# Optimization experiments

Hardware: AMD Instinct MI355X
Metric: run time of the kernel (lower is better)

The kernel has to match this reference:

```python
import jax, jax.numpy as jnp
import numpy as np

B, T, H = 2, 2048, 1024
EXPAND, N = 2, 16
DIN = H * EXPAND  # 2048
EPS = 1e-6


def rmsnorm(x, w):
    var = jnp.mean(x * x, axis=-1, keepdims=True)
    return x * jax.lax.rsqrt(var + EPS) * w


def setup_inputs() -> dict:
    key = jax.random.key(0)
    ks = jax.random.split(key, 9)
    s_h = 1.0 / np.sqrt(H)
    s_d = 1.0 / np.sqrt(DIN)
    return {
        "x": jax.random.normal(ks[0], (B, T, H), jnp.float32),
        "norm_w": jnp.ones((H,), jnp.float32),
        "in_proj_w": jax.random.normal(ks[1], (H, 2 * DIN), jnp.float32) * s_h,
        "A_proj_w": jax.random.normal(ks[2], (DIN, DIN), jnp.float32) * s_d,
        "A_proj_b": jax.random.normal(ks[3], (DIN,), jnp.float32) * 0.02,
        "A_base": jnp.log(jnp.arange(1, N + 1, dtype=jnp.float32)),
        "B_proj_w": jax.random.normal(ks[4], (DIN, N), jnp.float32) * s_d,
        "C_proj_w": jax.random.normal(ks[5], (DIN, N), jnp.float32) * s_d,
        "D": jnp.ones((DIN,), jnp.float32),
        "out_proj_w": jax.random.normal(ks[6], (DIN, H), jnp.float32) * s_d,
    }


def liquid_scan(x_in, a_mod, a_base, B_in, C_in):
    # x_in, a_mod: [B,T,DIN]; B_in, C_in: [B,T,N]; a_base: [N]
    def step(h, inp):
        a_t, b_t, c_t, x_t = inp  # [B,DIN], [B,N], [B,N], [B,DIN]
        # h: [B, DIN, N]
        h = (a_t[:, :, None] * a_base) * h + b_t[:, None, :] * x_t[:, :, None]
        y_t = jnp.einsum('bdn,bn->bd', h, c_t)
        return h, y_t

    h0 = jnp.zeros((x_in.shape[0], DIN, N), x_in.dtype)
    xs = (jnp.swapaxes(a_mod, 0, 1), jnp.swapaxes(B_in, 0, 1),
          jnp.swapaxes(C_in, 0, 1), jnp.swapaxes(x_in, 0, 1))
    _, ys = jax.lax.scan(step, h0, xs)  # ys: [T,B,DIN]
    return jnp.swapaxes(ys, 0, 1)


def reference(x, norm_w, in_proj_w, A_proj_w, A_proj_b, A_base, B_proj_w, C_proj_w, D, out_proj_w):
    residual = x
    xn = rmsnorm(x, norm_w)
    xz = xn @ in_proj_w                      # [B,T,2*DIN]
    x_in, z = jnp.split(xz, 2, axis=-1)
    x_in = jax.nn.silu(x_in)
    a_mod = jax.nn.sigmoid(x_in @ A_proj_w + A_proj_b)  # [B,T,DIN]
    a_base = jax.nn.sigmoid(A_base)                      # [N]
    B_in = x_in @ B_proj_w                               # [B,T,N]
    C_in = x_in @ C_proj_w                               # [B,T,N]
    y = liquid_scan(x_in, a_mod, a_base, B_in, C_in)     # [B,T,DIN]
    y = (y + D * x_in) * jax.nn.silu(z)
    return residual + y @ out_proj_w
```

## Files before the change

kernel.cpp:

```cpp
#include <hip/hip_runtime.h>
#include <hip/hip_fp16.h>
#include <cstdint>

#define B_    2
#define T_    2048
#define H_    1024
#define DIN_  2048
#define NS_   16
#define M_    (B_*T_)
#define NCHUNK 64
#define LCHUNK 32

using bf16x8 = __attribute__((ext_vector_type(8))) short;
using f32x4  = __attribute__((ext_vector_type(4))) float;

__device__ __forceinline__ unsigned short f2bf(float f) {
    union { float f; uint32_t u; } x; x.f = f;
    uint32_t u = x.u;
    uint32_t r = (u + 0x7fffu + ((u >> 16) & 1u)) >> 16;
    return (unsigned short)r;
}
__device__ __forceinline__ float bf2f(unsigned short h) {
    union { uint32_t u; float f; } x; x.u = ((uint32_t)h) << 16;
    return x.f;
}
__device__ __forceinline__ float sigm(float v) { return 1.0f / (1.0f + expf(-v)); }
__device__ __forceinline__ float silu(float v) { return v / (1.0f + expf(-v)); }

__device__ __forceinline__ void gload_lds16(const void* g, void* l) {
    __builtin_amdgcn_global_load_lds(
        (__attribute__((address_space(1))) void*)(void*)g,
        (__attribute__((address_space(3))) void*)l, 16, 0, 0);
}

__global__ __launch_bounds__(256)
void prep_all(const float* __restrict__ in_proj, const float* __restrict__ A_proj,
              const float* __restrict__ out_proj,
              const float* __restrict__ x, const float* __restrict__ norm_w,
              unsigned short* __restrict__ inT, unsigned short* __restrict__ W2,
              unsigned short* __restrict__ outT, unsigned short* __restrict__ xnh) {
    int bid = blockIdx.x;
    int tid = threadIdx.x;
    __shared__ float tile[32][33];
    __shared__ float red[4];
    if (bid >= 10240) {
        int row = bid - 10240;
        const float4* xr = (const float4*)(x + (size_t)row * H_);
        float4 v = xr[tid];
        float ss = v.x * v.x + v.y * v.y + v.z * v.z + v.w * v.w;
#pragma unroll
        for (int o = 32; o > 0; o >>= 1) ss += __shfl_down(ss, o, 64);
        int lane = tid & 63, wv = tid >> 6;
        if (lane == 0) red[wv] = ss;
        __syncthreads();
        float tot = red[0] + red[1] + red[2] + red[3];
        float rstd = rsqrtf(tot / (float)H_ + 1e-6f);
        const float4* wr = (const float4*)norm_w;
        float4 w4 = wr[tid];
        size_t o = (size_t)row * H_ + tid * 4;
        *(ushort4*)&xnh[o] = make_ushort4(f2bf(v.x * rstd * w4.x), f2bf(v.y * rstd * w4.y),
                                          f2bf(v.z * rstd * w4.z), f2bf(v.w * rstd * w4.w));
        return;
    }
    const float* src; unsigned short* dst; int K, N, l;
    if (bid < 4096)      { src = in_proj;  dst = inT;  K = 1024; N = 4096; l = bid; }
    else if (bid < 8192) { src = A_proj;   dst = W2;   K = 2048; N = 2048; l = bid - 4096; }
    else                 { src = out_proj; dst = outT; K = 2048; N = 1024; l = bid - 8192; }
    int ntiles = N >> 5;
    int n0 = (l % ntiles) * 32, k0 = (l / ntiles) * 32;
    int tx = tid & 31, ty = tid >> 5;
#pragma unroll
    for (int i = 0; i < 32; i += 8)
        tile[ty + i][tx] = src[(size_t)(k0 + ty + i) * N + (n0 + tx)];
    __syncthreads();
    int sx = (tid & 15) * 2;
    int sy = tid >> 4;
#pragma unroll
    for (int i = 0; i < 32; i += 16) {
        int n = sy + i;
        float v0 = tile[sx][n], v1 = tile[sx + 1][n];
        size_t o = (size_t)(n0 + n) * K + (k0 + sx);
        *(ushort2*)&dst[o] = make_ushort2(f2bf(v0), f2bf(v1));
    }
}

template <int EPI, int BM, int BN>
__global__ __launch_bounds__(512, (BM == 128) ? 4 : 2)
void gemm8p(const unsigned short* __restrict__ Aa, const unsigned short* __restrict__ Bw,
            int K,
            float* __restrict__ out0,
            unsigned short* __restrict__ oh, unsigned short* __restrict__ oz,
            const float* __restrict__ aux, __half* __restrict__ oha) {
    constexpr int AU   = (BM / 16) * 2;
    constexpr int BU   = (BN / 16) * 2;
    constexpr int BUFU = AU + BU;
    constexpr int MF   = BM / 2 / 16;
    constexpr int NF   = BN / 4 / 16;
    constexpr int PH   = (NF == 4) ? 2 : 1;
    constexpr int NP   = NF / PH;
    constexpr int SPWK = BUFU / 8;
    constexpr int SPG  = SPWK / 2;
    constexpr int SPP  = SPG / PH;
    __shared__ unsigned short sm[2 * BUFU * 512];
    const int tid  = threadIdx.x;
    const int lane = tid & 63;
    const int wid  = tid >> 6;
    const int wm   = wid >> 2;
    const int wn   = wid & 3;

    const int gx   = gridDim.x;
    const int nwg  = gx * gridDim.y;
    const int orig = blockIdx.y * gx + blockIdx.x;
    const int qq   = nwg >> 3;
    const int lid  = (orig & 7) * qq + (orig >> 3);
    const int bm   = (lid / gx) * BM;
    const int bn   = (lid % gx) * BN;

    const int srow  = lane >> 2;
    const int sgran = (lane & 3) ^ ((lane >> 3) & 3);
    const unsigned short* gpp[SPWK];
    int lofs_[SPWK];
#pragma unroll
    for (int g = 0; g < 2; ++g)
#pragma unroll
        for (int i = 0; i < SPG; ++i) {
            int cn = wid * SPG + i;
            const unsigned short* src;
            int u;
            if (cn < AU / 2) { u = cn * 2 + g;             src = Aa + (size_t)(bm + cn * 16 + srow) * K; }
            else { int bc = cn - AU / 2; u = AU + bc * 2 + g; src = Bw + (size_t)(bn + bc * 16 + srow) * K; }
            gpp[g * SPG + i]   = src + g * 32 + sgran * 8;
            lofs_[g * SPG + i] = u * 512;
        }

    const int nt = K >> 6;
#pragma unroll
    for (int j = 0; j < SPWK; ++j) gload_lds16(gpp[j], &sm[lofs_[j]]);

    const int fro = (lane & 15) * 32 + (((lane >> 4) ^ ((lane >> 1) & 3)) * 8);

    f32x4 acc[MF][NF] = {};
    for (int kt = 0; kt < nt; ++kt) {
        const unsigned short* sb = &sm[(kt & 1) * (BUFU * 512)];
        unsigned short*       db = &sm[((kt + 1) & 1) * (BUFU * 512)];
        const bool pf = (kt + 1 < nt);
        bf16x8 af[MF];
#pragma unroll
        for (int ks = 0; ks < 2; ++ks) {
            if (ks == 1 && kt == nt - 1) {
                asm volatile("s_waitcnt vmcnt(0)" ::: "memory");
            } else {
                if constexpr (SPG == 4)      asm volatile("s_waitcnt vmcnt(4)" ::: "memory");
                else if constexpr (SPG == 3) asm volatile("s_waitcnt vmcnt(3)" ::: "memory");
                else                         asm volatile("s_waitcnt vmcnt(2)" ::: "memory");
            }
            __builtin_amdgcn_s_barrier();
            __builtin_amdgcn_sched_barrier(0);
#pragma unroll
            for (int ph = 0; ph < PH; ++ph) {
                if (ph) {
                    __builtin_amdgcn_s_barrier();
                    __builtin_amdgcn_sched_barrier(0);
                }
                if (ph == 0) {
#pragma unroll
                    for (int mf = 0; mf < MF; ++mf)
                        af[mf] = *(const bf16x8*)&sb[((wm * MF + mf) * 2 + ks) * 512 + fro];
                }
                bf16x8 bf8[NP];
#pragma unroll
                for (int j = 0; j < NP; ++j) {
                    int nfg = ph * NP + j;
                    bf8[j] = *(const bf16x8*)&sb[(AU + (wn * NF + nfg) * 2 + ks) * 512 + fro];
                }
                if (pf) {
#pragma unroll
                    for (int j = 0; j < SPP; ++j) {
                        int s = (ks * PH + ph) * SPP + j;
                        gload_lds16(gpp[s] + (size_t)(kt + 1) * 64, db + lofs_[s]);
                    }
                }
                __builtin_amdgcn_s_setprio(1);
#pragma unroll
                for (int mf = 0; mf < MF; ++mf)
#pragma unroll
                    for (int j = 0; j < NP; ++j)
                        acc[mf][ph * NP + j] = __builtin_amdgcn_mfma_f32_16x16x32_bf16(
                            af[mf], bf8[j], acc[mf][ph * NP + j], 0, 0, 0);
                __builtin_amdgcn_s_setprio(0);
            }
        }
    }

#pragma unroll
    for (int mf = 0; mf < MF; ++mf)
#pragma unroll
        for (int nf = 0; nf < NF; ++nf) {
            int col  = bn + (wn * NF + nf) * 16 + (lane & 15);
            int row0 = bm + (wm * MF + mf) * 16 + ((lane >> 4) << 2);
#pragma unroll
            for (int r = 0; r < 4; ++r) {
                int row = row0 + r;
                float v = acc[mf][nf][r];
                if (EPI == 0) {
                    float s = silu(v);
                    if (col < DIN_) oh[(size_t)row * DIN_ + col] = f2bf(s);
                    else            oz[(size_t)row * DIN_ + (col - DIN_)] = f2bf(s);
                } else if (EPI == 1) {
                    oha[(size_t)row * DIN_ + col] = __float2half(sigm(v + aux[col]));
                } else {
                    out0[(size_t)row * H_ + col] = v + aux[(size_t)row * H_ + col];
                }
            }
        }
}

#define KT_ 512
__global__ __launch_bounds__(256)
void bc_proj(const unsigned short* __restrict__ xh,
             const float* __restrict__ Bw, const float* __restrict__ Cw,
             float* __restrict__ Bout, float* __restrict__ Cout) {
    __shared__ float wB[KT_][17];
    __shared__ float wC[KT_][17];
    const int m0  = blockIdx.x * 16;
    const int tid = threadIdx.x;
    const int r   = tid >> 4;
    const int j   = tid & 15;
    float ab[16], ac[16];
#pragma unroll
    for (int i = 0; i < 16; ++i) { ab[i] = 0.f; ac[i] = 0.f; }

    for (int kt = 0; kt < DIN_; kt += KT_) {
        if (kt) __syncthreads();
        const float4* bs = (const float4*)(Bw + (size_t)kt * 16);
        const float4* cs = (const float4*)(Cw + (size_t)kt * 16);
#pragma unroll
        for (int i = 0; i < 8; ++i) {
            int idx = i * 256 + tid;
            int kk = idx >> 2, c4 = (idx & 3) * 4;
            float4 vb = bs[idx], vc = cs[idx];
            wB[kk][c4 + 0] = vb.x; wB[kk][c4 + 1] = vb.y; wB[kk][c4 + 2] = vb.z; wB[kk][c4 + 3] = vb.w;
            wC[kk][c4 + 0] = vc.x; wC[kk][c4 + 1] = vc.y; wC[kk][c4 + 2] = vc.z; wC[kk][c4 + 3] = vc.w;
        }
        __syncthreads();
        const unsigned short* xr = xh + (size_t)(m0 + r) * DIN_ + kt;
#pragma unroll 4
        for (int kk = 0; kk < 32; ++kk) {
            int kl = kk * 16 + j;
            float x = bf2f(xr[kl]);
#pragma unroll
            for (int c = 0; c < 16; ++c) {
                ab[c] = fmaf(x, wB[kl][c], ab[c]);
                ac[c] = fmaf(x, wC[kl][c], ac[c]);
            }
        }
    }
#pragma unroll
    for (int i = 0; i < 16; ++i) {
#pragma unroll
        for (int m = 8; m > 0; m >>= 1) {
            ab[i] += __shfl_xor(ab[i], m, 64);
            ac[i] += __shfl_xor(ac[i], m, 64);
        }
    }
    if (j == 0) {
#pragma unroll
        for (int i = 0; i < 16; ++i) {
            Bout[(size_t)(m0 + r) * 16 + i] = ab[i];
            Cout[(size_t)(m0 + r) * 16 + i] = ac[i];
        }
    }
}

__global__ __launch_bounds__(256)
void scan_phase1(const __half* __restrict__ amod, const unsigned short* __restrict__ xh,
                 const float* __restrict__ Bin, const float* __restrict__ Abase,
                 float* __restrict__ P, float* __restrict__ S) {
    int d = blockIdx.x * 256 + threadIdx.x;
    int c = blockIdx.y;
    int b = blockIdx.z;
    float ab[16];
#pragma unroll
    for (int n = 0; n < 16; ++n) ab[n] = sigm(Abase[n]);
    float p[16], s[16];
#pragma unroll
    for (int n = 0; n < 16; ++n) { p[n] = 1.0f; s[n] = 0.0f; }
    int t0 = c * LCHUNK;
    for (int tt = 0; tt < LCHUNK; ++tt) {
        size_t mrow = (size_t)(b * T_ + t0 + tt);
        float a = __half2float(amod[mrow * DIN_ + d]);
        float x = bf2f(xh[mrow * DIN_ + d]);
        const float4* bt4 = (const float4*)(Bin + mrow * 16);
        float4 q0 = bt4[0], q1 = bt4[1], q2 = bt4[2], q3 = bt4[3];
        float bt[16];
        bt[0]=q0.x; bt[1]=q0.y; bt[2]=q0.z; bt[3]=q0.w;
        bt[4]=q1.x; bt[5]=q1.y; bt[6]=q1.z; bt[7]=q1.w;
        bt[8]=q2.x; bt[9]=q2.y; bt[10]=q2.z; bt[11]=q2.w;
        bt[12]=q3.x; bt[13]=q3.y; bt[14]=q3.z; bt[15]=q3.w;
#pragma unroll
        for (int n = 0; n < 16; ++n) {
            float dk = a * ab[n];
            p[n] *= dk;
            s[n] = fmaf(dk, s[n], bt[n] * x);
        }
    }
    size_t base = ((size_t)(b * NCHUNK + c) << 15) + (size_t)d * 16;
    float4* P4 = (float4*)(P + base);
    float4* S4 = (float4*)(S + base);
#pragma unroll
    for (int j = 0; j < 4; ++j) {
        P4[j] = make_float4(p[4*j], p[4*j+1], p[4*j+2], p[4*j+3]);
        S4[j] = make_float4(s[4*j], s[4*j+1], s[4*j+2], s[4*j+3]);
    }
}

__global__ __launch_bounds__(256)
void scan_phase2(const float* __restrict__ P, const float* __restrict__ S,
                 float* __restrict__ H0) {
    int idx = blockIdx.x * 256 + threadIdx.x;
    int b = idx >> 15;
    int dn = idx & 32767;
    float g = 0.f;
    for (int c = 0; c < NCHUNK; ++c) {
        size_t base = ((size_t)(b * NCHUNK + c) << 15) + dn;
        H0[base] = g;
        g = fmaf(P[base], g, S[base]);
    }
}

__global__ __launch_bounds__(256)
void scan_phase3(const __half* __restrict__ amod, const unsigned short* __restrict__ xh,
                 const float* __restrict__ Bin, const float* __restrict__ Cin,
                 const float* __restrict__ Abase, const float* __restrict__ H0,
                 const float* __restrict__ Dp, const unsigned short* __restrict__ szh,
                 unsigned short* __restrict__ yh) {
    int d = blockIdx.x * 256 + threadIdx.x;
    int c = blockIdx.y;
    int b = blockIdx.z;
    float ab[16];
#pragma unroll
    for (int n = 0; n < 16; ++n) ab[n] = sigm(Abase[n]);
    float h[16];
    size_t hbase = ((size_t)(b * NCHUNK + c) << 15) + (size_t)d * 16;
    const float4* H4 = (const float4*)(H0 + hbase);
#pragma unroll
    for (int j = 0; j < 4; ++j) {
        float4 t4 = H4[j];
        h[j*4] = t4.x; h[j*4+1] = t4.y; h[j*4+2] = t4.z; h[j*4+3] = t4.w;
    }
    float Dd = Dp[d];
    int t0 = c * LCHUNK;
    for (int tt = 0; tt < LCHUNK; ++tt) {
        size_t mrow = (size_t)(b * T_ + t0 + tt);
        float a = __half2float(amod[mrow * DIN_ + d]);
        float x = bf2f(xh[mrow * DIN_ + d]);
        const float4* bt4 = (const float4*)(Bin + mrow * 16);
        const float4* ct4 = (const float4*)(Cin + mrow * 16);
        float4 q0 = bt4[0], q1 = bt4[1], q2 = bt4[2], q3 = bt4[3];
        float4 r0 = ct4[0], r1 = ct4[1], r2 = ct4[2], r3 = ct4[3];
        float bt[16], ct[16];
        bt[0]=q0.x; bt[1]=q0.y; bt[2]=q0.z; bt[3]=q0.w;
        bt[4]=q1.x; bt[5]=q1.y; bt[6]=q1.z; bt[7]=q1.w;
        bt[8]=q2.x; bt[9]=q2.y; bt[10]=q2.z; bt[11]=q2.w;
        bt[12]=q3.x; bt[13]=q3.y; bt[14]=q3.z; bt[15]=q3.w;
        ct[0]=r0.x; ct[1]=r0.y; ct[2]=r0.z; ct[3]=r0.w;
        ct[4]=r1.x; ct[5]=r1.y; ct[6]=r1.z; ct[7]=r1.w;
        ct[8]=r2.x; ct[9]=r2.y; ct[10]=r2.z; ct[11]=r2.w;
        ct[12]=r3.x; ct[13]=r3.y; ct[14]=r3.z; ct[15]=r3.w;
        float y = 0.f;
#pragma unroll
        for (int n = 0; n < 16; ++n) {
            float dk = a * ab[n];
            h[n] = fmaf(dk, h[n], bt[n] * x);
            y = fmaf(h[n], ct[n], y);
        }
        float val = (y + Dd * x) * bf2f(szh[mrow * DIN_ + d]);
        yh[mrow * DIN_ + d] = f2bf(val);
    }
}

extern "C" void kernel_launch(void* const* d_in, const int* in_sizes, int n_in,
                              void* d_out, int out_size, void* d_ws, size_t ws_size,
                              hipStream_t stream) {
    const float* x          = (const float*)d_in[0];
    const float* norm_w     = (const float*)d_in[1];
    const float* in_proj_w  = (const float*)d_in[2];
    const float* A_proj_w   = (const float*)d_in[3];
    const float* A_proj_b   = (const float*)d_in[4];
    const float* A_base     = (const float*)d_in[5];
    const float* B_proj_w   = (const float*)d_in[6];
    const float* C_proj_w   = (const float*)d_in[7];
    const float* Dp         = (const float*)d_in[8];
    const float* out_proj_w = (const float*)d_in[9];
    float* out = (float*)d_out;

    char* ws = (char*)d_ws;
    size_t off = 0;
    auto alloc = [&](size_t bytes) -> char* {
        char* p = ws + off;
        off += (bytes + 255) & ~(size_t)255;
        return p;
    };
    unsigned short* inT  = (unsigned short*)alloc((size_t)4096 * 1024 * 2);
    unsigned short* W2   = (unsigned short*)alloc((size_t)2048 * 2048 * 2);
    unsigned short* outT = (unsigned short*)alloc((size_t)1024 * 2048 * 2);
    unsigned short* xnh  = (unsigned short*)alloc((size_t)M_ * H_ * 2);
    unsigned short* xinh = (unsigned short*)alloc((size_t)M_ * DIN_ * 2);
    unsigned short* szh  = (unsigned short*)alloc((size_t)M_ * DIN_ * 2);
    __half* amod  = (__half*)alloc((size_t)M_ * DIN_ * 2);
    float* Bin    = (float*)alloc((size_t)M_ * 16 * 4);
    float* Cin    = (float*)alloc((size_t)M_ * 16 * 4);
    float* Pw     = (float*)alloc((size_t)B_ * NCHUNK * DIN_ * NS_ * 4);
    float* Sw     = (float*)alloc((size_t)B_ * NCHUNK * DIN_ * NS_ * 4);
    float* H0w    = (float*)alloc((size_t)B_ * NCHUNK * DIN_ * NS_ * 4);
    unsigned short* yh = (unsigned short*)alloc((size_t)M_ * DIN_ * 2);
    (void)ws_size;

    prep_all<<<14336, 256, 0, stream>>>(in_proj_w, A_proj_w, out_proj_w, x, norm_w,
                                        inT, W2, outT, xnh);

    gemm8p<0, 256, 256><<<dim3(4096 / 256, M_ / 256), 512, 0, stream>>>(
        xnh, inT, 1024, nullptr, xinh, szh, nullptr, nullptr);

    gemm8p<1, 256, 128><<<dim3(2048 / 128, M_ / 256), 512, 0, stream>>>(
        xinh, W2, 2048, nullptr, nullptr, nullptr, A_proj_b, amod);

    bc_proj<<<M_ / 16, 256, 0, stream>>>(xinh, B_proj_w, C_proj_w, Bin, Cin);

    scan_phase1<<<dim3(DIN_ / 256, NCHUNK, B_), 256, 0, stream>>>(amod, xinh, Bin, A_base, Pw, Sw);
    scan_phase2<<<(B_ * DIN_ * NS_) / 256, 256, 0, stream>>>(Pw, Sw, H0w);
    scan_phase3<<<dim3(DIN_ / 256, NCHUNK, B_), 256, 0, stream>>>(
        amod, xinh, Bin, Cin, A_base, H0w, Dp, szh, yh);

    gemm8p<2, 128, 128><<<dim3(1024 / 128, M_ / 128), 512, 0, stream>>>(
        yh, outT, 2048, out, nullptr, nullptr, x, nullptr);
}
```

Baseline: 229.2 us.

## Parametrize GEMM warp grid and restructure LDS barrier/wait scheduling in main loop

Adds template parameters for the warp layout (MW x NW). The second GEMM now uses a 4x2 warp grid instead of 2x4, and the phase split is driven by MF*NF instead of NF. The K-loop is reordered so LDS fragment loads are issued first, then a barrier and lgkmcnt wait, then MFMAs, with the vmcnt wait and the next barrier moved to the end of each phase. This is meant to overlap global prefetch and LDS reads with compute better and to shorten the fragment-load wait before MFMAs. In exchange it adds barriers and changes the fragment register footprint.

Measured after the change: 232.9 us. Within noise of the previous version (+1.6%).

```diff
diff --git a/kernel.cpp b/kernel.cpp
--- a/kernel.cpp
+++ b/kernel.cpp
@@ -84,7 +84,7 @@
     }
 }
 
-template <int EPI, int BM, int BN>
+template <int EPI, int BM, int BN, int MW, int NW>
 __global__ __launch_bounds__(512, (BM == 128) ? 4 : 2)
 void gemm8p(const unsigned short* __restrict__ Aa, const unsigned short* __restrict__ Bw,
             int K,
@@ -94,10 +94,10 @@
     constexpr int AU   = (BM / 16) * 2;
     constexpr int BU   = (BN / 16) * 2;
     constexpr int BUFU = AU + BU;
-    constexpr int MF   = BM / 2 / 16;
-    constexpr int NF   = BN / 4 / 16;
-    constexpr int PH   = (NF == 4) ? 2 : 1;
-    constexpr int NP   = NF / PH;
+    constexpr int MF   = BM / MW / 16;
+    constexpr int NF   = BN / NW / 16;
+    constexpr int PH   = (MF * NF >= 32) ? 2 : 1;
+    constexpr int MFR  = MF / PH;
     constexpr int SPWK = BUFU / 8;
     constexpr int SPG  = SPWK / 2;
     constexpr int SPP  = SPG / PH;
@@ -105,8 +105,8 @@
     const int tid  = threadIdx.x;
     const int lane = tid & 63;
     const int wid  = tid >> 6;
-    const int wm   = wid >> 2;
-    const int wn   = wid & 3;
+    const int wm   = wid / NW;
+    const int wn   = wid % NW;
 
     const int gx   = gridDim.x;
     const int nwg  = gx * gridDim.y;
@@ -136,6 +136,10 @@
     const int nt = K >> 6;
 #pragma unroll
     for (int j = 0; j < SPWK; ++j) gload_lds16(gpp[j], &sm[lofs_[j]]);
+    if constexpr (SPG == 4)      asm volatile("s_waitcnt vmcnt(4)" ::: "memory");
+    else if constexpr (SPG == 3) asm volatile("s_waitcnt vmcnt(3)" ::: "memory");
+    else                         asm volatile("s_waitcnt vmcnt(2)" ::: "memory");
+    __builtin_amdgcn_s_barrier();
 
     const int fro = (lane & 15) * 32 + (((lane >> 4) ^ ((lane >> 1) & 3)) * 8);
 
@@ -144,34 +148,19 @@
         const unsigned short* sb = &sm[(kt & 1) * (BUFU * 512)];
         unsigned short*       db = &sm[((kt + 1) & 1) * (BUFU * 512)];
         const bool pf = (kt + 1 < nt);
-        bf16x8 af[MF];
 #pragma unroll
         for (int ks = 0; ks < 2; ++ks) {
-            if (ks == 1 && kt == nt - 1) {
-                asm volatile("s_waitcnt vmcnt(0)" ::: "memory");
-            } else {
-                if constexpr (SPG == 4)      asm volatile("s_waitcnt vmcnt(4)" ::: "memory");
-                else if constexpr (SPG == 3) asm volatile("s_waitcnt vmcnt(3)" ::: "memory");
-                else                         asm volatile("s_waitcnt vmcnt(2)" ::: "memory");
-            }
-            __builtin_amdgcn_s_barrier();
-            __builtin_amdgcn_sched_barrier(0);
+            bf16x8 bf8[NF];
 #pragma unroll
             for (int ph = 0; ph < PH; ++ph) {
-                if (ph) {
-                    __builtin_amdgcn_s_barrier();
-                    __builtin_amdgcn_sched_barrier(0);
-                }
+                bf16x8 af[MFR];
+#pragma unroll
+                for (int i = 0; i < MFR; ++i)
+                    af[i] = *(const bf16x8*)&sb[((wm * MF + ph * MFR + i) * 2 + ks) * 512 + fro];
                 if (ph == 0) {
 #pragma unroll
-                    for (int mf = 0; mf < MF; ++mf)
-                        af[mf] = *(const bf16x8*)&sb[((wm * MF + mf) * 2 + ks) * 512 + fro];
-                }
-                bf16x8 bf8[NP];
-#pragma unroll
-                for (int j = 0; j < NP; ++j) {
-                    int nfg = ph * NP + j;
-                    bf8[j] = *(const bf16x8*)&sb[(AU + (wn * NF + nfg) * 2 + ks) * 512 + fro];
+                    for (int nf = 0; nf < NF; ++nf)
+                        bf8[nf] = *(const bf16x8*)&sb[(AU + (wn * NF + nf) * 2 + ks) * 512 + fro];
                 }
                 if (pf) {
 #pragma unroll
@@ -180,14 +169,29 @@
                         gload_lds16(gpp[s] + (size_t)(kt + 1) * 64, db + lofs_[s]);
                     }
                 }
+                __builtin_amdgcn_sched_barrier(0);
+                __builtin_amdgcn_s_barrier();
+                asm volatile("s_waitcnt lgkmcnt(0)" ::: "memory");
+                __builtin_amdgcn_sched_barrier(0);
                 __builtin_amdgcn_s_setprio(1);
 #pragma unroll
-                for (int mf = 0; mf < MF; ++mf)
-#pragma unroll
-                    for (int j = 0; j < NP; ++j)
-                        acc[mf][ph * NP + j] = __builtin_amdgcn_mfma_f32_16x16x32_bf16(
-                            af[mf], bf8[j], acc[mf][ph * NP + j], 0, 0, 0);
+                for (int i = 0; i < MFR; ++i)
+#pragma unroll
+                    for (int nf = 0; nf < NF; ++nf)
+                        acc[ph * MFR + i][nf] = __builtin_amdgcn_mfma_f32_16x16x32_bf16(
+                            af[i], bf8[nf], acc[ph * MFR + i][nf], 0, 0, 0);
                 __builtin_amdgcn_s_setprio(0);
+                if (ph == PH - 1) {
+                    if (kt == nt - 1) {
+                        if (ks == 0) asm volatile("s_waitcnt vmcnt(0)" ::: "memory");
+                    } else {
+                        if constexpr (SPG == 4)      asm volatile("s_waitcnt vmcnt(4)" ::: "memory");
+                        else if constexpr (SPG == 3) asm volatile("s_waitcnt vmcnt(3)" ::: "memory");
+                        else                         asm volatile("s_waitcnt vmcnt(2)" ::: "memory");
+                    }
+                }
+                __builtin_amdgcn_sched_barrier(0);
+                __builtin_amdgcn_s_barrier();
             }
         }
     }
@@ -419,10 +423,10 @@
     prep_all<<<14336, 256, 0, stream>>>(in_proj_w, A_proj_w, out_proj_w, x, norm_w,
                                         inT, W2, outT, xnh);
 
-    gemm8p<0, 256, 256><<<dim3(4096 / 256, M_ / 256), 512, 0, stream>>>(
+    gemm8p<0, 256, 256, 2, 4><<<dim3(4096 / 256, M_ / 256), 512, 0, stream>>>(
         xnh, inT, 1024, nullptr, xinh, szh, nullptr, nullptr);
 
-    gemm8p<1, 256, 128><<<dim3(2048 / 128, M_ / 256), 512, 0, stream>>>(
+    gemm8p<1, 256, 128, 4, 2><<<dim3(2048 / 128, M_ / 256), 512, 0, stream>>>(
         xinh, W2, 2048, nullptr, nullptr, nullptr, A_proj_b, amod);
 
     bc_proj<<<M_ / 16, 256, 0, stream>>>(xinh, B_proj_w, C_proj_w, Bin, Cin);
@@ -432,6 +436,6 @@
     scan_phase3<<<dim3(DIN_ / 256, NCHUNK, B_), 256, 0, stream>>>(
         amod, xinh, Bin, Cin, A_base, H0w, Dp, szh, yh);
 
-    gemm8p<2, 128, 128><<<dim3(1024 / 128, M_ / 128), 512, 0, stream>>>(
+    gemm8p<2, 128, 128, 2, 4><<<dim3(1024 / 128, M_ / 128), 512, 0, stream>>>(
         yh, outT, 2048, out, nullptr, nullptr, x, nullptr);
 }
```

## Restructure GEMM main loop into register double-buffered two-phase pipeline

Applied to the files above, without the earlier changes.

Rewrites the bf16 MFMA GEMM inner loop so fragments for the next k-half are loaded from LDS into a second register set while MFMAs run on the current set. Global-to-LDS prefetch is split into two halves interleaved with the compute phases, with one barrier per half-step. The first projection GEMM also moves from 256x256 to 256x128 tiles, which doubles the grid. This aims to hide LDS read latency behind MFMA issue and cut barrier stalls, at the cost of more registers and the changed reuse pattern of the smaller tile.

Measured after the change: 243.8 us. 1.06x slower.

```diff
diff --git a/kernel.cpp b/kernel.cpp
--- a/kernel.cpp
+++ b/kernel.cpp
@@ -86,7 +86,7 @@
 
 template <int EPI, int BM, int BN>
 __global__ __launch_bounds__(512, (BM == 128) ? 4 : 2)
-void gemm8p(const unsigned short* __restrict__ Aa, const unsigned short* __restrict__ Bw,
+void gemm2p(const unsigned short* __restrict__ Aa, const unsigned short* __restrict__ Bw,
             int K,
             float* __restrict__ out0,
             unsigned short* __restrict__ oh, unsigned short* __restrict__ oz,
@@ -94,14 +94,12 @@
     constexpr int AU   = (BM / 16) * 2;
     constexpr int BU   = (BN / 16) * 2;
     constexpr int BUFU = AU + BU;
+    constexpr int BUFS = BUFU * 512;
     constexpr int MF   = BM / 2 / 16;
     constexpr int NF   = BN / 4 / 16;
-    constexpr int PH   = (NF == 4) ? 2 : 1;
-    constexpr int NP   = NF / PH;
     constexpr int SPWK = BUFU / 8;
     constexpr int SPG  = SPWK / 2;
-    constexpr int SPP  = SPG / PH;
-    __shared__ unsigned short sm[2 * BUFU * 512];
+    __shared__ __align__(16) unsigned short sm[2 * BUFS];
     const int tid  = threadIdx.x;
     const int lane = tid & 63;
     const int wid  = tid >> 6;
@@ -134,62 +132,81 @@
         }
 
     const int nt = K >> 6;
+    const int fro = (lane & 15) * 32 + (((lane >> 4) ^ ((lane >> 1) & 3)) * 8);
+
 #pragma unroll
     for (int j = 0; j < SPWK; ++j) gload_lds16(gpp[j], &sm[lofs_[j]]);
-
-    const int fro = (lane & 15) * 32 + (((lane >> 4) ^ ((lane >> 1) & 3)) * 8);
+    if constexpr (SPG == 3)      asm volatile("s_waitcnt vmcnt(3)" ::: "memory");
+    else if constexpr (SPG == 2) asm volatile("s_waitcnt vmcnt(2)" ::: "memory");
+    else                         asm volatile("s_waitcnt vmcnt(4)" ::: "memory");
+    __builtin_amdgcn_sched_barrier(0);
+    __builtin_amdgcn_s_barrier();
+    __builtin_amdgcn_sched_barrier(0);
+    bf16x8 afA[MF], bfA[NF], afB[MF], bfB[NF];
+#pragma unroll
+    for (int mf = 0; mf < MF; ++mf)
+        afA[mf] = *(const bf16x8*)&sm[((wm * MF + mf) * 2 + 0) * 512 + fro];
+#pragma unroll
+    for (int nf = 0; nf < NF; ++nf)
+        bfA[nf] = *(const bf16x8*)&sm[(AU + (wn * NF + nf) * 2 + 0) * 512 + fro];
 
     f32x4 acc[MF][NF] = {};
     for (int kt = 0; kt < nt; ++kt) {
-        const unsigned short* sb = &sm[(kt & 1) * (BUFU * 512)];
-        unsigned short*       db = &sm[((kt + 1) & 1) * (BUFU * 512)];
+        const int bc  = (kt & 1) * BUFS;
+        const int bn2 = ((kt + 1) & 1) * BUFS;
         const bool pf = (kt + 1 < nt);
-        bf16x8 af[MF];
-#pragma unroll
-        for (int ks = 0; ks < 2; ++ks) {
-            if (ks == 1 && kt == nt - 1) {
-                asm volatile("s_waitcnt vmcnt(0)" ::: "memory");
-            } else {
-                if constexpr (SPG == 4)      asm volatile("s_waitcnt vmcnt(4)" ::: "memory");
-                else if constexpr (SPG == 3) asm volatile("s_waitcnt vmcnt(3)" ::: "memory");
-                else                         asm volatile("s_waitcnt vmcnt(2)" ::: "memory");
-            }
-            __builtin_amdgcn_s_barrier();
-            __builtin_amdgcn_sched_barrier(0);
-#pragma unroll
-            for (int ph = 0; ph < PH; ++ph) {
-                if (ph) {
-                    __builtin_amdgcn_s_barrier();
-                    __builtin_amdgcn_sched_barrier(0);
-                }
-                if (ph == 0) {
-#pragma unroll
-                    for (int mf = 0; mf < MF; ++mf)
-                        af[mf] = *(const bf16x8*)&sb[((wm * MF + mf) * 2 + ks) * 512 + fro];
-                }
-                bf16x8 bf8[NP];
-#pragma unroll
-                for (int j = 0; j < NP; ++j) {
-                    int nfg = ph * NP + j;
-                    bf8[j] = *(const bf16x8*)&sb[(AU + (wn * NF + nfg) * 2 + ks) * 512 + fro];
-                }
-                if (pf) {
-#pragma unroll
-                    for (int j = 0; j < SPP; ++j) {
-                        int s = (ks * PH + ph) * SPP + j;
-                        gload_lds16(gpp[s] + (size_t)(kt + 1) * 64, db + lofs_[s]);
-                    }
-                }
-                __builtin_amdgcn_s_setprio(1);
-#pragma unroll
-                for (int mf = 0; mf < MF; ++mf)
-#pragma unroll
-                    for (int j = 0; j < NP; ++j)
-                        acc[mf][ph * NP + j] = __builtin_amdgcn_mfma_f32_16x16x32_bf16(
-                            af[mf], bf8[j], acc[mf][ph * NP + j], 0, 0, 0);
-                __builtin_amdgcn_s_setprio(0);
-            }
-        }
+        if (pf) {
+#pragma unroll
+            for (int j = 0; j < SPG; ++j)
+                gload_lds16(gpp[j] + (size_t)(kt + 1) * 64, &sm[bn2 + lofs_[j]]);
+            if constexpr (SPG == 3)      asm volatile("s_waitcnt vmcnt(3)" ::: "memory");
+            else if constexpr (SPG == 2) asm volatile("s_waitcnt vmcnt(2)" ::: "memory");
+            else                         asm volatile("s_waitcnt vmcnt(4)" ::: "memory");
+        } else {
+            asm volatile("s_waitcnt vmcnt(0)" ::: "memory");
+        }
+        __builtin_amdgcn_sched_barrier(0);
+        __builtin_amdgcn_s_barrier();
+        __builtin_amdgcn_sched_barrier(0);
+#pragma unroll
+        for (int mf = 0; mf < MF; ++mf)
+            afB[mf] = *(const bf16x8*)&sm[bc + ((wm * MF + mf) * 2 + 1) * 512 + fro];
+#pragma unroll
+        for (int nf = 0; nf < NF; ++nf)
+            bfB[nf] = *(const bf16x8*)&sm[bc + (AU + (wn * NF + nf) * 2 + 1) * 512 + fro];
+        __builtin_amdgcn_s_setprio(1);
+#pragma unroll
+        for (int mf = 0; mf < MF; ++mf)
+#pragma unroll
+            for (int nf = 0; nf < NF; ++nf)
+                acc[mf][nf] = __builtin_amdgcn_mfma_f32_16x16x32_bf16(afA[mf], bfA[nf], acc[mf][nf], 0, 0, 0);
+        __builtin_amdgcn_s_setprio(0);
+        if (pf) {
+#pragma unroll
+            for (int j = SPG; j < SPWK; ++j)
+                gload_lds16(gpp[j] + (size_t)(kt + 1) * 64, &sm[bn2 + lofs_[j]]);
+            if constexpr (SPG == 3)      asm volatile("s_waitcnt vmcnt(3)" ::: "memory");
+            else if constexpr (SPG == 2) asm volatile("s_waitcnt vmcnt(2)" ::: "memory");
+            else                         asm volatile("s_waitcnt vmcnt(4)" ::: "memory");
+        }
+        __builtin_amdgcn_sched_barrier(0);
+        __builtin_amdgcn_s_barrier();
+        __builtin_amdgcn_sched_barrier(0);
+        if (pf) {
+#pragma unroll
+            for (int mf = 0; mf < MF; ++mf)
+                afA[mf] = *(const bf16x8*)&sm[bn2 + ((wm * MF + mf) * 2 + 0) * 512 + fro];
+#pragma unroll
+            for (int nf = 0; nf < NF; ++nf)
+                bfA[nf] = *(const bf16x8*)&sm[bn2 + (AU + (wn * NF + nf) * 2 + 0) * 512 + fro];
+        }
+        __builtin_amdgcn_s_setprio(1);
+#pragma unroll
+        for (int mf = 0; mf < MF; ++mf)
+#pragma unroll
+            for (int nf = 0; nf < NF; ++nf)
+                acc[mf][nf] = __builtin_amdgcn_mfma_f32_16x16x32_bf16(afB[mf], bfB[nf], acc[mf][nf], 0, 0, 0);
+        __builtin_amdgcn_s_setprio(0);
     }
 
 #pragma unroll
@@ -419,10 +436,10 @@
     prep_all<<<14336, 256, 0, stream>>>(in_proj_w, A_proj_w, out_proj_w, x, norm_w,
                                         inT, W2, outT, xnh);
 
-    gemm8p<0, 256, 256><<<dim3(4096 / 256, M_ / 256), 512, 0, stream>>>(
+    gemm2p<0, 256, 128><<<dim3(4096 / 128, M_ / 256), 512, 0, stream>>>(
         xnh, inT, 1024, nullptr, xinh, szh, nullptr, nullptr);
 
-    gemm8p<1, 256, 128><<<dim3(2048 / 128, M_ / 256), 512, 0, stream>>>(
+    gemm2p<1, 256, 128><<<dim3(2048 / 128, M_ / 256), 512, 0, stream>>>(
         xinh, W2, 2048, nullptr, nullptr, nullptr, A_proj_b, amod);
 
     bc_proj<<<M_ / 16, 256, 0, stream>>>(xinh, B_proj_w, C_proj_w, Bin, Cin);
@@ -432,6 +449,6 @@
     scan_phase3<<<dim3(DIN_ / 256, NCHUNK, B_), 256, 0, stream>>>(
         amod, xinh, Bin, Cin, A_base, H0w, Dp, szh, yh);
 
-    gemm8p<2, 128, 128><<<dim3(1024 / 128, M_ / 128), 512, 0, stream>>>(
+    gemm2p<2, 128, 128><<<dim3(1024 / 128, M_ / 128), 512, 0, stream>>>(
         yh, outT, 2048, out, nullptr, nullptr, x, nullptr);
 }
```

## Split-K the output projection GEMM into two halves plus reduction kernel

Applied to the files above, without the earlier changes.

The final out_proj GEMM is launched with a third grid dimension of 2, so each half of the K range runs in its own set of workgroups and writes fp32 partials into scratch buffers (Pw, and the next buffer reached past its end). A new elementwise kernel then sums the residual and the two partials into the output. The goal is to double the workgroup count, since the previous 256-tile launch underfills the GPU. The cost is writing and re-reading two full fp32 partial matrices plus an extra launch. It also assumes the second partial lands in Sw because the workspace buffers are contiguous.

Result: slower. 241.0 us (+5.1%).

```diff
diff --git a/kernel.cpp b/kernel.cpp
--- a/kernel.cpp
+++ b/kernel.cpp
@@ -87,7 +87,7 @@
 template <int EPI, int BM, int BN>
 __global__ __launch_bounds__(512, (BM == 128) ? 4 : 2)
 void gemm8p(const unsigned short* __restrict__ Aa, const unsigned short* __restrict__ Bw,
-            int K,
+            int K, int LDK,
             float* __restrict__ out0,
             unsigned short* __restrict__ oh, unsigned short* __restrict__ oz,
             const float* __restrict__ aux, __half* __restrict__ oha) {
@@ -108,6 +108,12 @@
     const int wm   = wid >> 2;
     const int wn   = wid & 3;
 
+    if (EPI == 3) {
+        int koff = blockIdx.z * K;
+        Aa += koff; Bw += koff;
+        out0 += (size_t)blockIdx.z * M_ * H_;
+    }
+
     const int gx   = gridDim.x;
     const int nwg  = gx * gridDim.y;
     const int orig = blockIdx.y * gx + blockIdx.x;
@@ -127,8 +133,8 @@
             int cn = wid * SPG + i;
             const unsigned short* src;
             int u;
-            if (cn < AU / 2) { u = cn * 2 + g;             src = Aa + (size_t)(bm + cn * 16 + srow) * K; }
-            else { int bc = cn - AU / 2; u = AU + bc * 2 + g; src = Bw + (size_t)(bn + bc * 16 + srow) * K; }
+            if (cn < AU / 2) { u = cn * 2 + g;             src = Aa + (size_t)(bm + cn * 16 + srow) * LDK; }
+            else { int bc = cn - AU / 2; u = AU + bc * 2 + g; src = Bw + (size_t)(bn + bc * 16 + srow) * LDK; }
             gpp[g * SPG + i]   = src + g * 32 + sgran * 8;
             lofs_[g * SPG + i] = u * 512;
         }
@@ -208,11 +214,24 @@
                     else            oz[(size_t)row * DIN_ + (col - DIN_)] = f2bf(s);
                 } else if (EPI == 1) {
                     oha[(size_t)row * DIN_ + col] = __float2half(sigm(v + aux[col]));
+                } else if (EPI == 2) {
+                    out0[(size_t)row * H_ + col] = v + aux[(size_t)row * H_ + col];
                 } else {
-                    out0[(size_t)row * H_ + col] = v + aux[(size_t)row * H_ + col];
+                    out0[(size_t)row * H_ + col] = v;
                 }
             }
         }
+}
+
+__global__ __launch_bounds__(256)
+void reduce_out(const float* __restrict__ x, const float* __restrict__ p0,
+                const float* __restrict__ p1, float* __restrict__ out) {
+    int i = blockIdx.x * 256 + threadIdx.x;
+    float4 a = ((const float4*)x)[i];
+    float4 b = ((const float4*)p0)[i];
+    float4 c = ((const float4*)p1)[i];
+    ((float4*)out)[i] = make_float4(a.x + b.x + c.x, a.y + b.y + c.y,
+                                    a.z + b.z + c.z, a.w + b.w + c.w);
 }
 
 #define KT_ 512
@@ -420,10 +439,10 @@
                                         inT, W2, outT, xnh);
 
     gemm8p<0, 256, 256><<<dim3(4096 / 256, M_ / 256), 512, 0, stream>>>(
-        xnh, inT, 1024, nullptr, xinh, szh, nullptr, nullptr);
+        xnh, inT, 1024, 1024, nullptr, xinh, szh, nullptr, nullptr);
 
     gemm8p<1, 256, 128><<<dim3(2048 / 128, M_ / 256), 512, 0, stream>>>(
-        xinh, W2, 2048, nullptr, nullptr, nullptr, A_proj_b, amod);
+        xinh, W2, 2048, 2048, nullptr, nullptr, nullptr, A_proj_b, amod);
 
     bc_proj<<<M_ / 16, 256, 0, stream>>>(xinh, B_proj_w, C_proj_w, Bin, Cin);
 
@@ -432,6 +451,8 @@
     scan_phase3<<<dim3(DIN_ / 256, NCHUNK, B_), 256, 0, stream>>>(
         amod, xinh, Bin, Cin, A_base, H0w, Dp, szh, yh);
 
-    gemm8p<2, 128, 128><<<dim3(1024 / 128, M_ / 128), 512, 0, stream>>>(
-        yh, outT, 2048, out, nullptr, nullptr, x, nullptr);
-}
+    gemm8p<3, 128, 128><<<dim3(1024 / 128, M_ / 128, 2), 512, 0, stream>>>(
+        yh, outT, 1024, 2048, Pw, nullptr, nullptr, nullptr, nullptr);
+
+    reduce_out<<<(M_ * H_ / 4) / 256, 256, 0, stream>>>(x, Pw, Sw, out);
+}
```
